# Kernel tuning notes

Hardware: AMD Instinct MI355X
Metric: run time of the kernel (lower is better)

The kernel has to match this reference:

```python
import jax, jax.numpy as jnp
import numpy as np

JITTER = 1e-05
TOL = 1e-04
MAX_ITER = 10
TAYLOR_ORDER = 5


def _safe_eigh(A):
    # torch safe_eigh: first attempt always adds jitter*I (eigh on SPD never fails, so first try succeeds)
    D = A.shape[-1]
    return jnp.linalg.eigh(A + JITTER * jnp.eye(D, dtype=A.dtype))


def _rebuild(vecs, vals):
    # vecs @ diag(vals) @ vecs^T, batched
    return jnp.einsum('...ij,...j,...kj->...ik', vecs, vals, vecs)


def matrix_sqrt(A):
    vals, vecs = _safe_eigh(A)
    return _rebuild(vecs, jnp.sqrt(jnp.clip(vals, JITTER)))


def matrix_inv_sqrt(A):
    vals, vecs = _safe_eigh(A)
    return _rebuild(vecs, 1.0 / jnp.sqrt(jnp.clip(vals, JITTER)))


def enforce_spd(M):
    vals, vecs = _safe_eigh(M)
    M2 = _rebuild(vecs, jnp.clip(vals, JITTER))
    return (M2 + jnp.swapaxes(M2, -1, -2)) * 0.5


def expm_taylor(Xm):
    D = Xm.shape[-1]
    I = jnp.broadcast_to(jnp.eye(D, dtype=Xm.dtype), Xm.shape)
    out = I
    Xp = I
    fac = 1.0
    for i in range(1, TAYLOR_ORDER + 1):
        Xp = Xp @ Xm
        fac *= i
        out = out + Xp / fac
    return out


def karcher_mean(X):
    # X: (B, N, D, D) SPD matrices -> (B, D, D) Riemannian (Karcher) mean
    B, N, D, _ = X.shape
    G0 = X.mean(axis=1)

    def step(carry, _):
        G, done = carry
        G_sqrt = matrix_sqrt(G)
        G_is = matrix_inv_sqrt(G)
        # A[b,n] = G_is[b] @ X[b,n] @ G_is[b]
        A = jnp.einsum('bij,bnjk,bkl->bnil', G_is, X, G_is)
        vals, vecs = _safe_eigh(A)
        logA = _rebuild(vecs, jnp.log(jnp.clip(vals, JITTER)))  # (B,N,D,D)
        Delta = logA.mean(axis=1)  # (B,D,D)
        norm_Delta = jnp.sqrt(jnp.sum(Delta * Delta, axis=(-2, -1))).mean()
        G_new = enforce_spd(G_sqrt @ expm_taylor(Delta) @ G_sqrt)
        # torch updates G, THEN checks break -> freeze only once done was set in a previous iter
        G_next = jnp.where(done, G, G_new)
        done_next = jnp.logical_or(done, norm_Delta < TOL)
        return (G_next, done_next), None

    (G, _), _ = jax.lax.scan(step, (G0, jnp.array(False)), None, length=MAX_ITER)
    return G


def setup_inputs() -> dict:
    key = jax.random.key(0)
    B, N, D = 64, 512, 32
    A = jax.random.normal(key, (B, N, D, D), dtype=jnp.float32)
    # well-conditioned SPD inputs, as an SPD pooling layer would receive
    X = A @ jnp.swapaxes(A, -1, -2) / D + 0.5 * jnp.eye(D, dtype=jnp.float32)
    return {"X": X}


def reference(X) -> jnp.ndarray:
    return karcher_mean(X)
```

## Files before the change

kernel.cpp:

```cpp
#include <hip/hip_runtime.h>
#include <math.h>

#define BB 64
#define NN 512
#define DD 32
#define LD2 36
#define LDG 32
#define JIT 1e-5f
#define TOLF 1e-4f
#define MAXIT 10

__device__ __forceinline__ float bpf(int addr, float v) {
    return __int_as_float(__builtin_amdgcn_ds_bpermute(addr, __float_as_int(v)));
}

__device__ __forceinline__ float swz16(float x) {
    return __int_as_float(__builtin_amdgcn_ds_swizzle(__float_as_int(x), 0x401F));
}

__device__ __forceinline__ float xhsum(float x) {
    unsigned u = __float_as_uint(x);
    auto r = __builtin_amdgcn_permlane32_swap(u, u, false, false);
    return __uint_as_float(r[0]) + __uint_as_float(r[1]);
}

__device__ __forceinline__ float xhmax(float x) {
    unsigned u = __float_as_uint(x);
    auto r = __builtin_amdgcn_permlane32_swap(u, u, false, false);
    return fmaxf(__uint_as_float(r[0]), __uint_as_float(r[1]));
}

__device__ __forceinline__ void wsync() {
    __asm__ volatile("s_waitcnt lgkmcnt(0)" ::: "memory");
}

template<int CTRL>
__device__ __forceinline__ float dppf(float x) {
    int i = __float_as_int(x);
    return __int_as_float(__builtin_amdgcn_update_dpp(i, i, CTRL, 0xF, 0xF, true));
}

__device__ __forceinline__ float part16(float x, bool hi16) {
#if __has_builtin(__builtin_amdgcn_permlane16_swap)
    unsigned u = __float_as_uint(x);
    auto r = __builtin_amdgcn_permlane16_swap(u, u, false, false);
    return hi16 ? __uint_as_float(r[0]) : __uint_as_float(r[1]);
#else
    return swz16(x);
#endif
}

__device__ __forceinline__ float max16pair(float x) {
#if __has_builtin(__builtin_amdgcn_permlane16_swap)
    unsigned u = __float_as_uint(x);
    auto r = __builtin_amdgcn_permlane16_swap(u, u, false, false);
    return fmaxf(__uint_as_float(r[0]), __uint_as_float(r[1]));
#else
    return fmaxf(x, swz16(x));
#endif
}

template<int LOW>
__device__ __forceinline__ float xorlane_lo(float x) {
    float v = x;
    if constexpr (LOW == 1)  v = dppf<0xB1>(v);
    else if constexpr (LOW == 2)  v = dppf<0x4E>(v);
    else if constexpr (LOW == 3)  v = dppf<0x1B>(v);
    else if constexpr (LOW == 4)  { v = dppf<0x141>(v); v = dppf<0x1B>(v); }
    else if constexpr (LOW == 5)  { v = dppf<0x141>(v); v = dppf<0x4E>(v); }
    else if constexpr (LOW == 6)  { v = dppf<0x141>(v); v = dppf<0xB1>(v); }
    else if constexpr (LOW == 7)  v = dppf<0x141>(v);
    else if constexpr (LOW == 8)  v = dppf<0x128>(v);
    else if constexpr (LOW == 9)  { v = dppf<0x128>(v); v = dppf<0xB1>(v); }
    else if constexpr (LOW == 10) { v = dppf<0x128>(v); v = dppf<0x4E>(v); }
    else if constexpr (LOW == 11) { v = dppf<0x128>(v); v = dppf<0x1B>(v); }
    else if constexpr (LOW == 12) { v = dppf<0x140>(v); v = dppf<0x1B>(v); }
    else if constexpr (LOW == 13) { v = dppf<0x140>(v); v = dppf<0x4E>(v); }
    else if constexpr (LOW == 14) { v = dppf<0x140>(v); v = dppf<0xB1>(v); }
    else if constexpr (LOW == 15) v = dppf<0x140>(v);
    return v;
}

__device__ __forceinline__ float redmax32(float x) {
    x = fmaxf(x, dppf<0xB1>(x));
    x = fmaxf(x, dppf<0x4E>(x));
    x = fmaxf(x, dppf<0x124>(x));
    x = fmaxf(x, dppf<0x128>(x));
    x = max16pair(x);
    return xhmax(x);
}

template<int M>
__device__ __forceinline__ void rot32(float a[32], int c, bool hi16, float& maxrel) {
    constexpr int LOW = M & 15;
    float pa[32];
#pragma unroll
    for (int i = 0; i < 32; ++i) {
        float t = xorlane_lo<LOW>(a[i]);
        if constexpr (M >= 16) pa[i] = (i < 16) ? swz16(t) : part16(t, hi16);
        else                   pa[i] = t;
    }
    float gs = 0.f, gc = 0.f;
#pragma unroll
    for (int i = 0; i < 32; ++i) {
        gs = fmaf(a[i], a[i], gs);
        gc = fmaf(a[i], pa[i], gc);
    }
    float gp;
    if constexpr (M < 16) gp = xorlane_lo<LOW>(gs);
    else                  gp = swz16(xorlane_lo<LOW>(gs));
    bool isP = c < (c ^ M);
    float gpp = isP ? gs : gp;
    float gqq = isP ? gp : gs;
    float rel = gc * gc * __builtin_amdgcn_rcpf(gpp * gqq);
    maxrel = fmaxf(maxrel, rel);
    float tau = (gqq - gpp) * (0.5f * __builtin_amdgcn_rcpf(gc));
    float den = fabsf(tau) + __builtin_amdgcn_sqrtf(fmaf(tau, tau, 1.f));
    float tt  = copysignf(__builtin_amdgcn_rcpf(den), tau);
    tt = (rel > 1e-24f) ? tt : 0.f;
    float cs  = __builtin_amdgcn_rsqf(fmaf(tt, tt, 1.f));
    float sn  = tt * cs;
    float sg = isP ? -sn : sn;
#pragma unroll
    for (int i = 0; i < 32; ++i) a[i] = fmaf(sg, pa[i], cs * a[i]);
}

__device__ __forceinline__ void jac_pair(float a[32], int c, bool hi16,
                                         int maxsweep, float thr) {
#pragma unroll 1
    for (int sweep = 0; sweep < maxsweep; ++sweep) {
        float maxrel = 0.f;
        rot32<1>(a, c, hi16, maxrel);  rot32<2>(a, c, hi16, maxrel);
        rot32<3>(a, c, hi16, maxrel);  rot32<4>(a, c, hi16, maxrel);
        rot32<5>(a, c, hi16, maxrel);  rot32<6>(a, c, hi16, maxrel);
        rot32<7>(a, c, hi16, maxrel);  rot32<8>(a, c, hi16, maxrel);
        rot32<9>(a, c, hi16, maxrel);  rot32<10>(a, c, hi16, maxrel);
        rot32<11>(a, c, hi16, maxrel); rot32<12>(a, c, hi16, maxrel);
        rot32<13>(a, c, hi16, maxrel); rot32<14>(a, c, hi16, maxrel);
        rot32<15>(a, c, hi16, maxrel); rot32<16>(a, c, hi16, maxrel);
        rot32<17>(a, c, hi16, maxrel); rot32<18>(a, c, hi16, maxrel);
        rot32<19>(a, c, hi16, maxrel); rot32<20>(a, c, hi16, maxrel);
        rot32<21>(a, c, hi16, maxrel); rot32<22>(a, c, hi16, maxrel);
        rot32<23>(a, c, hi16, maxrel); rot32<24>(a, c, hi16, maxrel);
        rot32<25>(a, c, hi16, maxrel); rot32<26>(a, c, hi16, maxrel);
        rot32<27>(a, c, hi16, maxrel); rot32<28>(a, c, hi16, maxrel);
        rot32<29>(a, c, hi16, maxrel); rot32<30>(a, c, hi16, maxrel);
        rot32<31>(a, c, hi16, maxrel);
        maxrel = redmax32(maxrel);
        if (maxrel < thr) break;
    }
}

__device__ __forceinline__ void mm32w(const float* A, const float* B, float* C, int lane) {
    int r = lane >> 1, cb = (lane & 1) << 4;
    float acc[16];
#pragma unroll
    for (int j = 0; j < 16; ++j) acc[j] = 0.0f;
    for (int k = 0; k < DD; ++k) {
        float a = A[r * LD2 + k];
        const float4* Br = (const float4*)(B + k * LD2 + cb);
        float4 b0 = Br[0], b1 = Br[1], b2 = Br[2], b3 = Br[3];
        acc[0]  = fmaf(a, b0.x, acc[0]);  acc[1]  = fmaf(a, b0.y, acc[1]);
        acc[2]  = fmaf(a, b0.z, acc[2]);  acc[3]  = fmaf(a, b0.w, acc[3]);
        acc[4]  = fmaf(a, b1.x, acc[4]);  acc[5]  = fmaf(a, b1.y, acc[5]);
        acc[6]  = fmaf(a, b1.z, acc[6]);  acc[7]  = fmaf(a, b1.w, acc[7]);
        acc[8]  = fmaf(a, b2.x, acc[8]);  acc[9]  = fmaf(a, b2.y, acc[9]);
        acc[10] = fmaf(a, b2.z, acc[10]); acc[11] = fmaf(a, b2.w, acc[11]);
        acc[12] = fmaf(a, b3.x, acc[12]); acc[13] = fmaf(a, b3.y, acc[13]);
        acc[14] = fmaf(a, b3.z, acc[14]); acc[15] = fmaf(a, b3.w, acc[15]);
    }
    wsync();
    float4* Cr = (float4*)(C + r * LD2 + cb);
    Cr[0] = make_float4(acc[0],  acc[1],  acc[2],  acc[3]);
    Cr[1] = make_float4(acc[4],  acc[5],  acc[6],  acc[7]);
    Cr[2] = make_float4(acc[8],  acc[9],  acc[10], acc[11]);
    Cr[3] = make_float4(acc[12], acc[13], acc[14], acc[15]);
    wsync();
}


__global__ __launch_bounds__(256) void k0_zero(float* __restrict__ G, int* __restrict__ done,
                                               float* __restrict__ norm_acc, int* __restrict__ cnt_all,
                                               int* __restrict__ cnt_b) {
    float4* Gb = (float4*)(G + blockIdx.x * 1024);
    Gb[threadIdx.x] = make_float4(0.f, 0.f, 0.f, 0.f);
    if (blockIdx.x == 0) {
        if (threadIdx.x == 0) { *done = 0; *norm_acc = 0.f; *cnt_all = 0; }
        if (threadIdx.x < BB) cnt_b[threadIdx.x] = 0;
    }
}

__global__ __launch_bounds__(256) void k0_mean(const float* __restrict__ X, float* __restrict__ G) {
    int blk = blockIdx.x;
    int b = blk >> 3, chunk = blk & 7;
    int t = threadIdx.x;
    const float4* Xb = (const float4*)(X + ((size_t)(b * NN + chunk * 64)) * 1024);
    float4 acc = make_float4(0.f, 0.f, 0.f, 0.f);
    for (int n = 0; n < 64; ++n) {
        float4 v = Xb[n * 256 + t];
        acc.x += v.x; acc.y += v.y; acc.z += v.z; acc.w += v.w;
    }
    const float inv = 1.0f / NN;
    float* Gb = G + b * 1024 + t * 4;
    atomicAdd(Gb + 0, acc.x * inv);
    atomicAdd(Gb + 1, acc.y * inv);
    atomicAdd(Gb + 2, acc.z * inv);
    atomicAdd(Gb + 3, acc.w * inv);
}


__global__ __launch_bounds__(64) void k1_init(const float* __restrict__ G,
                                              float* __restrict__ Gs, float* __restrict__ Gis,
                                              float* __restrict__ Vg) {
    int b = blockIdx.x, lane = threadIdx.x;
    int c = lane & 31;
    bool hi16 = (lane & 16) != 0;
    int r = lane >> 1, cb = (lane & 1) << 4;
    __shared__ __align__(16) float sW[DD * LD2];
    __shared__ float sc1[DD], sc2[DD];

    float a[32];
    {
        const float4* Gc = (const float4*)(G + b * 1024 + c * 32);
#pragma unroll
        for (int j4 = 0; j4 < 8; ++j4) {
            float4 q = Gc[j4];
            a[4*j4] = q.x; a[4*j4+1] = q.y; a[4*j4+2] = q.z; a[4*j4+3] = q.w;
        }
        a[c] += JIT;
    }
    jac_pair(a, c, hi16, 10, 1e-12f);
    float gs2 = 0.f;
#pragma unroll
    for (int i = 0; i < 32; ++i) gs2 = fmaf(a[i], a[i], gs2);
    float l  = __builtin_amdgcn_sqrtf(gs2);
    float lc = fmaxf(l, JIT);
    float ig = __builtin_amdgcn_rcpf(gs2);
    float c1 = __builtin_amdgcn_sqrtf(lc) * ig;
    float c2 = __builtin_amdgcn_rsqf(lc) * ig;
    if (Vg && lane < 32) {
        float inl = __builtin_amdgcn_rsqf(gs2);
        float4* Vp = (float4*)(Vg + b * 1024 + c * 32);
#pragma unroll
        for (int j4 = 0; j4 < 8; ++j4)
            Vp[j4] = make_float4(a[4*j4]*inl, a[4*j4+1]*inl, a[4*j4+2]*inl, a[4*j4+3]*inl);
    }
    if (lane < 32) {
        float4* wp = (float4*)&sW[c * LD2];
#pragma unroll
        for (int j4 = 0; j4 < 8; ++j4)
            wp[j4] = make_float4(a[4*j4], a[4*j4+1], a[4*j4+2], a[4*j4+3]);
        sc1[c] = c1; sc2[c] = c2;
    }
    wsync();
    float a1[16], a2[16];
#pragma unroll
    for (int j = 0; j < 16; ++j) { a1[j] = 0.f; a2[j] = 0.f; }
    for (int k = 0; k < DD; ++k) {
        float wr = sW[k * LD2 + r];
        float t1 = wr * sc1[k], t2 = wr * sc2[k];
        const float4* Wc = (const float4*)&sW[k * LD2 + cb];
        float4 w0 = Wc[0], w1 = Wc[1], w2 = Wc[2], w3 = Wc[3];
        a1[0]+=t1*w0.x; a2[0]+=t2*w0.x;  a1[1]+=t1*w0.y; a2[1]+=t2*w0.y;
        a1[2]+=t1*w0.z; a2[2]+=t2*w0.z;  a1[3]+=t1*w0.w; a2[3]+=t2*w0.w;
        a1[4]+=t1*w1.x; a2[4]+=t2*w1.x;  a1[5]+=t1*w1.y; a2[5]+=t2*w1.y;
        a1[6]+=t1*w1.z; a2[6]+=t2*w1.z;  a1[7]+=t1*w1.w; a2[7]+=t2*w1.w;
        a1[8]+=t1*w2.x; a2[8]+=t2*w2.x;  a1[9]+=t1*w2.y; a2[9]+=t2*w2.y;
        a1[10]+=t1*w2.z; a2[10]+=t2*w2.z; a1[11]+=t1*w2.w; a2[11]+=t2*w2.w;
        a1[12]+=t1*w3.x; a2[12]+=t2*w3.x; a1[13]+=t1*w3.y; a2[13]+=t2*w3.y;
        a1[14]+=t1*w3.z; a2[14]+=t2*w3.z; a1[15]+=t1*w3.w; a2[15]+=t2*w3.w;
    }
    float4* Gsb  = (float4*)(Gs  + b * 1024 + lane * 16);
    float4* Gisb = (float4*)(Gis + b * 1024 + lane * 16);
#pragma unroll
    for (int j4 = 0; j4 < 4; ++j4) {
        Gsb[j4]  = make_float4(a1[4*j4], a1[4*j4+1], a1[4*j4+2], a1[4*j4+3]);
        Gisb[j4] = make_float4(a2[4*j4], a2[4*j4+1], a2[4*j4+2], a2[4*j4+3]);
    }
}


__global__ __launch_bounds__(512, 4) void k2_log_acc(const float* __restrict__ X,
                                                     float* G, float* Gs, float* Gis,
                                                     float* __restrict__ Part,
                                                     int* __restrict__ done,
                                                     float* __restrict__ Vbuf,
                                                     float* __restrict__ Vg,
                                                     float* __restrict__ norm_acc,
                                                     int* __restrict__ cnt_all,
                                                     int* __restrict__ cnt_b,
                                                     int it) {
    if (*done) return;
    int b = blockIdx.x >> 4, grp = blockIdx.x & 15;
    int wv = threadIdx.x >> 6, lane = threadIdx.x & 63;
    int c = lane & 31, h = lane >> 5;
    bool hi16 = (lane & 16) != 0;
    int aself = lane << 2;

    __shared__ __align__(16) float sG[DD * LDG];
    __shared__ __align__(16) float sAall[8][DD * LD2];
    float* sA = sAall[wv];

    if (threadIdx.x < 256)
        ((float4*)sG)[threadIdx.x] = ((const float4*)(Gis + b * 1024))[threadIdx.x];
    __syncthreads();

    int r = lane >> 1, cb = (lane & 1) << 4;
    float dacc[16];
#pragma unroll
    for (int j = 0; j < 16; ++j) dacc[j] = 0.f;

#pragma unroll 1
    for (int pp = 0; pp < 2; ++pp) {
        int nb = grp * 32 + wv * 4 + pp * 2;
        float a[32];
#pragma unroll 1
        for (int half = 0; half < 2; ++half) {
            int n = nb + half;
            {
                const float4* Xv = (const float4*)(X + ((size_t)(b * NN + n)) * 1024);
                float4 v0 = Xv[lane * 4 + 0], v1 = Xv[lane * 4 + 1];
                float4 v2 = Xv[lane * 4 + 2], v3 = Xv[lane * 4 + 3];
                wsync();
                int e = lane * 16;
                float* d0 = &sA[(e >> 5) * LD2 + (e & 31)];
                *((float4*)d0)        = v0;
                *((float4*)(d0 + 4))  = v1;
                *((float4*)(d0 + 8))  = v2;
                *((float4*)(d0 + 12)) = v3;
                wsync();
            }
            {
                float acc[16];
#pragma unroll
                for (int j = 0; j < 16; ++j) acc[j] = 0.f;
                for (int k = 0; k < DD; ++k) {
                    float av = sG[k * LDG + r];
                    const float4* Br = (const float4*)(sA + k * LD2 + cb);
                    float4 b0 = Br[0], b1 = Br[1], b2 = Br[2], b3 = Br[3];
                    acc[0]  = fmaf(av, b0.x, acc[0]);  acc[1]  = fmaf(av, b0.y, acc[1]);
                    acc[2]  = fmaf(av, b0.z, acc[2]);  acc[3]  = fmaf(av, b0.w, acc[3]);
                    acc[4]  = fmaf(av, b1.x, acc[4]);  acc[5]  = fmaf(av, b1.y, acc[5]);
                    acc[6]  = fmaf(av, b1.z, acc[6]);  acc[7]  = fmaf(av, b1.w, acc[7]);
                    acc[8]  = fmaf(av, b2.x, acc[8]);  acc[9]  = fmaf(av, b2.y, acc[9]);
                    acc[10] = fmaf(av, b2.z, acc[10]); acc[11] = fmaf(av, b2.w, acc[11]);
                    acc[12] = fmaf(av, b3.x, acc[12]); acc[13] = fmaf(av, b3.y, acc[13]);
                    acc[14] = fmaf(av, b3.z, acc[14]); acc[15] = fmaf(av, b3.w, acc[15]);
                }
                wsync();
                float4* Cr = (float4*)(sA + r * LD2 + cb);
                Cr[0] = make_float4(acc[0],  acc[1],  acc[2],  acc[3]);
                Cr[1] = make_float4(acc[4],  acc[5],  acc[6],  acc[7]);
                Cr[2] = make_float4(acc[8],  acc[9],  acc[10], acc[11]);
                Cr[3] = make_float4(acc[12], acc[13], acc[14], acc[15]);
                wsync();
            }
            {
                float acc[16];
#pragma unroll
                for (int j = 0; j < 16; ++j) acc[j] = 0.f;
                for (int k = 0; k < DD; ++k) {
                    float av = sA[r * LD2 + k];
                    const float4* Br = (const float4*)(sG + k * LDG + cb);
                    float4 b0 = Br[0], b1 = Br[1], b2 = Br[2], b3 = Br[3];
                    acc[0]  = fmaf(av, b0.x, acc[0]);  acc[1]  = fmaf(av, b0.y, acc[1]);
                    acc[2]  = fmaf(av, b0.z, acc[2]);  acc[3]  = fmaf(av, b0.w, acc[3]);
                    acc[4]  = fmaf(av, b1.x, acc[4]);  acc[5]  = fmaf(av, b1.y, acc[5]);
                    acc[6]  = fmaf(av, b1.z, acc[6]);  acc[7]  = fmaf(av, b1.w, acc[7]);
                    acc[8]  = fmaf(av, b2.x, acc[8]);  acc[9]  = fmaf(av, b2.y, acc[9]);
                    acc[10] = fmaf(av, b2.z, acc[10]); acc[11] = fmaf(av, b2.w, acc[11]);
                    acc[12] = fmaf(av, b3.x, acc[12]); acc[13] = fmaf(av, b3.y, acc[13]);
                    acc[14] = fmaf(av, b3.z, acc[14]); acc[15] = fmaf(av, b3.w, acc[15]);
                }
                wsync();
                float4* Cr = (float4*)(sA + r * LD2 + cb);
                Cr[0] = make_float4(acc[0],  acc[1],  acc[2],  acc[3]);
                Cr[1] = make_float4(acc[4],  acc[5],  acc[6],  acc[7]);
                Cr[2] = make_float4(acc[8],  acc[9],  acc[10], acc[11]);
                Cr[3] = make_float4(acc[12], acc[13], acc[14], acc[15]);
                wsync();
            }
            if (h == half) {
                if (it == 0) {
                    float tr[32];
                    const float4* rp = (const float4*)&sA[c * LD2];
#pragma unroll
                    for (int j4 = 0; j4 < 8; ++j4) {
                        float4 q = rp[j4];
                        tr[4*j4]=q.x; tr[4*j4+1]=q.y; tr[4*j4+2]=q.z; tr[4*j4+3]=q.w;
                    }
#pragma unroll
                    for (int i = 0; i < 32; ++i) {
                        float v = 0.5f * (sA[i * LD2 + c] + tr[i]);
                        a[i] = (i == c) ? (tr[i] + JIT) : v;
                    }
                } else {
                    float v[32];
                    const float4* Vp = (const float4*)(Vbuf + ((size_t)(b * NN + n)) * 1024 + c * 32);
#pragma unroll
                    for (int j4 = 0; j4 < 8; ++j4) {
                        float4 t = Vp[j4];
                        v[4*j4]=t.x; v[4*j4+1]=t.y; v[4*j4+2]=t.z; v[4*j4+3]=t.w;
                    }
#pragma unroll
                    for (int i = 0; i < 32; ++i) {
                        const float4* Ar = (const float4*)&sA[i * LD2];
                        float s = 0.f;
#pragma unroll
                        for (int j4 = 0; j4 < 8; ++j4) {
                            float4 q = Ar[j4];
                            s = fmaf(q.x, v[4*j4],   s);
                            s = fmaf(q.y, v[4*j4+1], s);
                            s = fmaf(q.z, v[4*j4+2], s);
                            s = fmaf(q.w, v[4*j4+3], s);
                        }
                        a[i] = fmaf(JIT, v[i], s);
                    }
                }
            }
        }

        jac_pair(a, c, hi16, 8, 1e-8f);

        float gs2 = 0.f;
#pragma unroll
        for (int i = 0; i < 32; ++i) gs2 = fmaf(a[i], a[i], gs2);
        float gs2c = fmaxf(gs2, JIT * JIT);
        float tk = 0.5f * logf(gs2c) * __builtin_amdgcn_rcpf(gs2);
        if (Vbuf) {
            int n = nb + h;
            float inl = __builtin_amdgcn_rsqf(gs2);
            float4* Vp = (float4*)(Vbuf + ((size_t)(b * NN + n)) * 1024 + c * 32);
#pragma unroll
            for (int j4 = 0; j4 < 8; ++j4)
                Vp[j4] = make_float4(a[4*j4]*inl, a[4*j4+1]*inl, a[4*j4+2]*inl, a[4*j4+3]*inl);
        }
#pragma unroll 1
        for (int half = 0; half < 2; ++half) {
            wsync();
            if (h == half) {
                float4* wp = (float4*)&sA[c * LD2];
#pragma unroll
                for (int j4 = 0; j4 < 8; ++j4)
                    wp[j4] = make_float4(a[4*j4], a[4*j4+1], a[4*j4+2], a[4*j4+3]);
                sA[c * LD2 + 32] = tk;
            }
            wsync();
            for (int k = 0; k < DD; ++k) {
                float t1 = sA[k * LD2 + r] * sA[k * LD2 + 32];
                const float4* Wr = (const float4*)&sA[k * LD2 + cb];
                float4 w0 = Wr[0], w1 = Wr[1], w2 = Wr[2], w3 = Wr[3];
                dacc[0]  = fmaf(t1, w0.x, dacc[0]);  dacc[1]  = fmaf(t1, w0.y, dacc[1]);
                dacc[2]  = fmaf(t1, w0.z, dacc[2]);  dacc[3]  = fmaf(t1, w0.w, dacc[3]);
                dacc[4]  = fmaf(t1, w1.x, dacc[4]);  dacc[5]  = fmaf(t1, w1.y, dacc[5]);
                dacc[6]  = fmaf(t1, w1.z, dacc[6]);  dacc[7]  = fmaf(t1, w1.w, dacc[7]);
                dacc[8]  = fmaf(t1, w2.x, dacc[8]);  dacc[9]  = fmaf(t1, w2.y, dacc[9]);
                dacc[10] = fmaf(t1, w2.z, dacc[10]); dacc[11] = fmaf(t1, w2.w, dacc[11]);
                dacc[12] = fmaf(t1, w3.x, dacc[12]); dacc[13] = fmaf(t1, w3.y, dacc[13]);
                dacc[14] = fmaf(t1, w3.z, dacc[14]); dacc[15] = fmaf(t1, w3.w, dacc[15]);
            }
        }
    }
    wsync();

    {
        float4* fp = (float4*)&sA[lane * 16];
        fp[0] = make_float4(dacc[0],  dacc[1],  dacc[2],  dacc[3]);
        fp[1] = make_float4(dacc[4],  dacc[5],  dacc[6],  dacc[7]);
        fp[2] = make_float4(dacc[8],  dacc[9],  dacc[10], dacc[11]);
        fp[3] = make_float4(dacc[12], dacc[13], dacc[14], dacc[15]);
    }
    __syncthreads();
    if (threadIdx.x < 256) {
        int t = threadIdx.x;
        float4 s0 = ((float4*)sAall[0])[t];
        float4 s1 = ((float4*)sAall[1])[t];
        float4 s2 = ((float4*)sAall[2])[t];
        float4 s3 = ((float4*)sAall[3])[t];
        float4 s4 = ((float4*)sAall[4])[t];
        float4 s5 = ((float4*)sAall[5])[t];
        float4 s6 = ((float4*)sAall[6])[t];
        float4 s7 = ((float4*)sAall[7])[t];
        float4 s;
        s.x = ((s0.x + s1.x) + (s2.x + s3.x)) + ((s4.x + s5.x) + (s6.x + s7.x));
        s.y = ((s0.y + s1.y) + (s2.y + s3.y)) + ((s4.y + s5.y) + (s6.y + s7.y));
        s.z = ((s0.z + s1.z) + (s2.z + s3.z)) + ((s4.z + s5.z) + (s6.z + s7.z));
        s.w = ((s0.w + s1.w) + (s2.w + s3.w)) + ((s4.w + s5.w) + (s6.w + s7.w));
        ((float4*)(Part + (size_t)blockIdx.x * 1024))[t] = s;
    }

    int* winp = (int*)sG;
    if (threadIdx.x == 0) *winp = 0;
    __syncthreads();
    if (threadIdx.x == 0) {
        __threadfence();
        int ret = atomicAdd(&cnt_b[b], 1);
        if (ret == 15) { *winp = 1; cnt_b[b] = 0; }
    }
    __syncthreads();
    if (*winp == 0) return;
    if (threadIdx.x >= 64) return;
    __threadfence();

    {
        float* s0 = sAall[0];
        float* s1 = sAall[1];
        float* s2 = sAall[2];
        float* scof = sAall[3];

        float d[16];
#pragma unroll
        for (int j = 0; j < 16; ++j) d[j] = 0.f;
#pragma unroll 1
        for (int g = 0; g < 16; ++g) {
            const float4* P = (const float4*)(Part + (size_t)(b * 16 + g) * 1024 + lane * 16);
            float4 p0 = P[0], p1 = P[1], p2 = P[2], p3 = P[3];
            d[0]+=p0.x; d[1]+=p0.y; d[2]+=p0.z; d[3]+=p0.w;
            d[4]+=p1.x; d[5]+=p1.y; d[6]+=p1.z; d[7]+=p1.w;
            d[8]+=p2.x; d[9]+=p2.y; d[10]+=p2.z; d[11]+=p2.w;
            d[12]+=p3.x; d[13]+=p3.y; d[14]+=p3.z; d[15]+=p3.w;
        }
        const float inv = 1.0f / NN;
        float sumsq = 0.f;
#pragma unroll
        for (int j = 0; j < 16; ++j) { d[j] *= inv; sumsq = fmaf(d[j], d[j], sumsq); }
#pragma unroll
        for (int sh = 1; sh <= 16; sh <<= 1) sumsq += bpf(aself ^ (sh << 2), sumsq);
        sumsq = xhsum(sumsq);
        if (lane == 0) atomicAdd(norm_acc, sqrtf(sumsq));

        wsync();
        {
            float4* dp = (float4*)&s0[r * LD2 + cb];
            dp[0] = make_float4(d[0],  d[1],  d[2],  d[3]);
            dp[1] = make_float4(d[4],  d[5],  d[6],  d[7]);
            dp[2] = make_float4(d[8],  d[9],  d[10], d[11]);
            dp[3] = make_float4(d[12], d[13], d[14], d[15]);
        }
        wsync();

        float outr[16];
#pragma unroll
        for (int j = 0; j < 16; ++j)
            outr[j] = ((cb + j) == r ? 1.0f : 0.0f) + d[j];
        float fac = 1.0f;
#pragma unroll 1
        for (int i = 2; i <= 5; ++i) {
            fac *= (float)i;
            float acc[16];
#pragma unroll
            for (int j = 0; j < 16; ++j) acc[j] = 0.f;
            const float* Xp = (i == 2) ? s0 : s1;
            for (int k = 0; k < DD; ++k) {
                float av = Xp[r * LD2 + k];
                const float4* Br = (const float4*)&s0[k * LD2 + cb];
                float4 b0 = Br[0], b1 = Br[1], b2 = Br[2], b3 = Br[3];
                acc[0]+=av*b0.x; acc[1]+=av*b0.y; acc[2]+=av*b0.z; acc[3]+=av*b0.w;
                acc[4]+=av*b1.x; acc[5]+=av*b1.y; acc[6]+=av*b1.z; acc[7]+=av*b1.w;
                acc[8]+=av*b2.x; acc[9]+=av*b2.y; acc[10]+=av*b2.z; acc[11]+=av*b2.w;
                acc[12]+=av*b3.x; acc[13]+=av*b3.y; acc[14]+=av*b3.z; acc[15]+=av*b3.w;
            }
            float invf = 1.0f / fac;
#pragma unroll
            for (int j = 0; j < 16; ++j) outr[j] = fmaf(acc[j], invf, outr[j]);
            wsync();
            float4* dp = (float4*)&s1[r * LD2 + cb];
            dp[0] = make_float4(acc[0],  acc[1],  acc[2],  acc[3]);
            dp[1] = make_float4(acc[4],  acc[5],  acc[6],  acc[7]);
            dp[2] = make_float4(acc[8],  acc[9],  acc[10], acc[11]);
            dp[3] = make_float4(acc[12], acc[13], acc[14], acc[15]);
            wsync();
        }
        {
            float4* dp = (float4*)&s0[r * LD2 + cb];
            dp[0] = make_float4(outr[0],  outr[1],  outr[2],  outr[3]);
            dp[1] = make_float4(outr[4],  outr[5],  outr[6],  outr[7]);
            dp[2] = make_float4(outr[8],  outr[9],  outr[10], outr[11]);
            dp[3] = make_float4(outr[12], outr[13], outr[14], outr[15]);
            const float4* Gsb = (const float4*)(Gs + b * 1024);
#pragma unroll
            for (int j4 = 0; j4 < 4; ++j4) {
                float4 v = Gsb[lane * 4 + j4];
                int e = lane * 16 + j4 * 4;
                *((float4*)&s1[(e >> 5) * LD2 + (e & 31)]) = v;
            }
        }
        wsync();
        mm32w(s1, s0, s2, lane);
        mm32w(s2, s1, s0, lane);

        float aa[32];
        if (Vg == nullptr) {
            float tr[32];
            const float4* rp = (const float4*)&s0[c * LD2];
#pragma unroll
            for (int j4 = 0; j4 < 8; ++j4) {
                float4 q = rp[j4];
                tr[4*j4]=q.x; tr[4*j4+1]=q.y; tr[4*j4+2]=q.z; tr[4*j4+3]=q.w;
            }
#pragma unroll
            for (int i = 0; i < 32; ++i) {
                float v = 0.5f * (s0[i * LD2 + c] + tr[i]);
                aa[i] = (i == c) ? (tr[i] + JIT) : v;
            }
        } else {
            float v[32];
            const float4* Vp = (const float4*)(Vg + b * 1024 + c * 32);
#pragma unroll
            for (int j4 = 0; j4 < 8; ++j4) {
                float4 t = Vp[j4];
                v[4*j4]=t.x; v[4*j4+1]=t.y; v[4*j4+2]=t.z; v[4*j4+3]=t.w;
            }
#pragma unroll
            for (int i = 0; i < 32; ++i) {
                const float4* Mr = (const float4*)&s0[i * LD2];
                float s = 0.f;
#pragma unroll
                for (int j4 = 0; j4 < 8; ++j4) {
                    float4 q = Mr[j4];
                    s = fmaf(q.x, v[4*j4],   s);
                    s = fmaf(q.y, v[4*j4+1], s);
                    s = fmaf(q.z, v[4*j4+2], s);
                    s = fmaf(q.w, v[4*j4+3], s);
                }
                aa[i] = fmaf(JIT, v[i], s);
            }
        }
        jac_pair(aa, c, hi16, 10, 1e-12f);
        float gs2 = 0.f;
#pragma unroll
        for (int i = 0; i < 32; ++i) gs2 = fmaf(aa[i], aa[i], gs2);
        float l = __builtin_amdgcn_sqrtf(gs2);
        float clipl = fmaxf(l, JIT);
        float ig = __builtin_amdgcn_rcpf(gs2);
        float tg = clipl * ig;
        float sh = clipl + JIT;
        float ts = __builtin_amdgcn_sqrtf(sh) * ig;
        float ti = __builtin_amdgcn_rsqf(sh) * ig;
        if (Vg && lane < 32) {
            float inl = __builtin_amdgcn_rsqf(gs2);
            float4* Vp = (float4*)(Vg + b * 1024 + c * 32);
#pragma unroll
            for (int j4 = 0; j4 < 8; ++j4)
                Vp[j4] = make_float4(aa[4*j4]*inl, aa[4*j4+1]*inl, aa[4*j4+2]*inl, aa[4*j4+3]*inl);
        }
        wsync();
        if (lane < 32) {
            float4* wp = (float4*)&s1[c * LD2];
#pragma unroll
            for (int j4 = 0; j4 < 8; ++j4)
                wp[j4] = make_float4(aa[4*j4], aa[4*j4+1], aa[4*j4+2], aa[4*j4+3]);
            scof[c] = tg; scof[32 + c] = ts; scof[64 + c] = ti;
        }
        wsync();
#pragma unroll 1
        for (int pass = 0; pass < 3; ++pass) {
            float g[16];
#pragma unroll
            for (int j = 0; j < 16; ++j) g[j] = 0.f;
            for (int k = 0; k < DD; ++k) {
                float t1 = s1[k * LD2 + r] * scof[pass * 32 + k];
                const float4* Wc = (const float4*)&s1[k * LD2 + cb];
                float4 w0 = Wc[0], w1 = Wc[1], w2 = Wc[2], w3 = Wc[3];
                g[0]+=t1*w0.x; g[1]+=t1*w0.y; g[2]+=t1*w0.z; g[3]+=t1*w0.w;
                g[4]+=t1*w1.x; g[5]+=t1*w1.y; g[6]+=t1*w1.z; g[7]+=t1*w1.w;
                g[8]+=t1*w2.x; g[9]+=t1*w2.y; g[10]+=t1*w2.z; g[11]+=t1*w2.w;
                g[12]+=t1*w3.x; g[13]+=t1*w3.y; g[14]+=t1*w3.z; g[15]+=t1*w3.w;
            }
            float* dst = (pass == 0) ? G : (pass == 1) ? Gs : Gis;
            float4* Db = (float4*)(dst + b * 1024 + lane * 16);
#pragma unroll
            for (int j4 = 0; j4 < 4; ++j4)
                Db[j4] = make_float4(g[4*j4], g[4*j4+1], g[4*j4+2], g[4*j4+3]);
        }

        __threadfence();
        if (lane == 0) {
            int r2 = atomicAdd(cnt_all, 1);
            if (r2 == BB - 1) {
                float nm = atomicAdd(norm_acc, 0.f);
                if (nm * (1.0f / BB) < TOLF) *done = 1;
                *norm_acc = 0.f;
                *cnt_all = 0;
                __threadfence();
            }
        }
    }
}

__global__ __launch_bounds__(256) void k5_out(const float* __restrict__ G, float* __restrict__ out) {
    int i = blockIdx.x * 256 + threadIdx.x;
    out[i] = G[i];
}

extern "C" void kernel_launch(void* const* d_in, const int* in_sizes, int n_in,
                              void* d_out, int out_size, void* d_ws, size_t ws_size,
                              hipStream_t stream) {
    const float* X = (const float*)d_in[0];
    float* ws = (float*)d_ws;
    float* G     = ws;
    float* Gs    = ws + 65536;
    float* Gis   = ws + 2 * 65536;
    float* Part  = ws + 3 * 65536;
    float* norm_acc = ws + 3 * 65536 + 1048576;
    int*   cnt_all  = (int*)(norm_acc + 1);
    int*   done     = (int*)(norm_acc + 2);
    int*   cnt_b    = (int*)(norm_acc + 3);
    size_t base_floats = (size_t)3 * 65536 + 1048576 + 80;
    float* Vg   = (ws_size >= (base_floats + (size_t)BB * 1024) * sizeof(float))
                  ? (ws + base_floats) : nullptr;
    float* Vbuf = (ws_size >= (base_floats + (size_t)BB * 1024 + (size_t)BB * NN * 1024) * sizeof(float))
                  ? (ws + base_floats + (size_t)BB * 1024) : nullptr;

    k0_zero<<<64, 256, 0, stream>>>(G, done, norm_acc, cnt_all, cnt_b);
    k0_mean<<<512, 256, 0, stream>>>(X, G);
    k1_init<<<64, 64, 0, stream>>>(G, Gs, Gis, Vg);
    for (int it = 0; it < MAXIT; ++it) {
        int it_eff = (Vbuf != nullptr) ? it : 0;
        k2_log_acc<<<1024, 512, 0, stream>>>(X, G, Gs, Gis, Part, done, Vbuf, Vg,
                                             norm_acc, cnt_all, cnt_b, it_eff);
    }
    k5_out<<<256, 256, 0, stream>>>(G, (float*)d_out);
}
```

Before: 4.455 ms.

## Replace pairwise Jacobi with round-robin quad layout using packed FMA

Rewrites the one-sided Jacobi eigen-solver so that each 16-lane group holds two columns (U,V) of a 32x32 matrix and rotates them with packed float2 FMAs. Columns then shift between lanes in a round-robin tournament via DPP, instead of each lane holding one column and fetching its partner across the full wave. This lets a 64-lane wave process four matrices at once (four samples per wave in k2) rather than two, and removes the costly cross-half permutes. In exchange it adds a dynamic 31-round loop, lane-select overhead, and a changed occupancy hint on the main kernel.

```diff
diff --git a/kernel.cpp b/kernel.cpp
--- a/kernel.cpp
+++ b/kernel.cpp
@@ -10,6 +10,12 @@
 #define TOLF 1e-4f
 #define MAXIT 10
 
+typedef float float2v __attribute__((ext_vector_type(2)));
+
+__device__ __forceinline__ float2v efma(float2v a, float2v b, float2v c) {
+    return __builtin_elementwise_fma(a, b, c);
+}
+
 __device__ __forceinline__ float bpf(int addr, float v) {
     return __int_as_float(__builtin_amdgcn_ds_bpermute(addr, __float_as_int(v)));
 }
@@ -38,16 +44,6 @@
 __device__ __forceinline__ float dppf(float x) {
     int i = __float_as_int(x);
     return __int_as_float(__builtin_amdgcn_update_dpp(i, i, CTRL, 0xF, 0xF, true));
-}
-
-__device__ __forceinline__ float part16(float x, bool hi16) {
-#if __has_builtin(__builtin_amdgcn_permlane16_swap)
-    unsigned u = __float_as_uint(x);
-    auto r = __builtin_amdgcn_permlane16_swap(u, u, false, false);
-    return hi16 ? __uint_as_float(r[0]) : __uint_as_float(r[1]);
-#else
-    return swz16(x);
-#endif
 }
 
 __device__ __forceinline__ float max16pair(float x) {
@@ -60,27 +56,6 @@
 #endif
 }
 
-template<int LOW>
-__device__ __forceinline__ float xorlane_lo(float x) {
-    float v = x;
-    if constexpr (LOW == 1)  v = dppf<0xB1>(v);
-    else if constexpr (LOW == 2)  v = dppf<0x4E>(v);
-    else if constexpr (LOW == 3)  v = dppf<0x1B>(v);
-    else if constexpr (LOW == 4)  { v = dppf<0x141>(v); v = dppf<0x1B>(v); }
-    else if constexpr (LOW == 5)  { v = dppf<0x141>(v); v = dppf<0x4E>(v); }
-    else if constexpr (LOW == 6)  { v = dppf<0x141>(v); v = dppf<0xB1>(v); }
-    else if constexpr (LOW == 7)  v = dppf<0x141>(v);
-    else if constexpr (LOW == 8)  v = dppf<0x128>(v);
-    else if constexpr (LOW == 9)  { v = dppf<0x128>(v); v = dppf<0xB1>(v); }
-    else if constexpr (LOW == 10) { v = dppf<0x128>(v); v = dppf<0x4E>(v); }
-    else if constexpr (LOW == 11) { v = dppf<0x128>(v); v = dppf<0x1B>(v); }
-    else if constexpr (LOW == 12) { v = dppf<0x140>(v); v = dppf<0x1B>(v); }
-    else if constexpr (LOW == 13) { v = dppf<0x140>(v); v = dppf<0x4E>(v); }
-    else if constexpr (LOW == 14) { v = dppf<0x140>(v); v = dppf<0xB1>(v); }
-    else if constexpr (LOW == 15) v = dppf<0x140>(v);
-    return v;
-}
-
 __device__ __forceinline__ float redmax32(float x) {
     x = fmaxf(x, dppf<0xB1>(x));
     x = fmaxf(x, dppf<0x4E>(x));
@@ -90,62 +65,59 @@
     return xhmax(x);
 }
 
-template<int M>
-__device__ __forceinline__ void rot32(float a[32], int c, bool hi16, float& maxrel) {
-    constexpr int LOW = M & 15;
-    float pa[32];
-#pragma unroll
-    for (int i = 0; i < 32; ++i) {
-        float t = xorlane_lo<LOW>(a[i]);
-        if constexpr (M >= 16) pa[i] = (i < 16) ? swz16(t) : part16(t, hi16);
-        else                   pa[i] = t;
-    }
-    float gs = 0.f, gc = 0.f;
-#pragma unroll
-    for (int i = 0; i < 32; ++i) {
-        gs = fmaf(a[i], a[i], gs);
-        gc = fmaf(a[i], pa[i], gc);
-    }
-    float gp;
-    if constexpr (M < 16) gp = xorlane_lo<LOW>(gs);
-    else                  gp = swz16(xorlane_lo<LOW>(gs));
-    bool isP = c < (c ^ M);
-    float gpp = isP ? gs : gp;
-    float gqq = isP ? gp : gs;
-    float rel = gc * gc * __builtin_amdgcn_rcpf(gpp * gqq);
-    maxrel = fmaxf(maxrel, rel);
-    float tau = (gqq - gpp) * (0.5f * __builtin_amdgcn_rcpf(gc));
-    float den = fabsf(tau) + __builtin_amdgcn_sqrtf(fmaf(tau, tau, 1.f));
-    float tt  = copysignf(__builtin_amdgcn_rcpf(den), tau);
-    tt = (rel > 1e-24f) ? tt : 0.f;
-    float cs  = __builtin_amdgcn_rsqf(fmaf(tt, tt, 1.f));
-    float sn  = tt * cs;
-    float sg = isP ? -sn : sn;
-#pragma unroll
-    for (int i = 0; i < 32; ++i) a[i] = fmaf(sg, pa[i], cs * a[i]);
-}
-
-__device__ __forceinline__ void jac_pair(float a[32], int c, bool hi16,
+__device__ __forceinline__ void jac_quad(float2v U[16], float2v V[16],
+                                         bool isL0, bool isL1, bool isL15,
                                          int maxsweep, float thr) {
 #pragma unroll 1
     for (int sweep = 0; sweep < maxsweep; ++sweep) {
         float maxrel = 0.f;
-        rot32<1>(a, c, hi16, maxrel);  rot32<2>(a, c, hi16, maxrel);
-        rot32<3>(a, c, hi16, maxrel);  rot32<4>(a, c, hi16, maxrel);
-        rot32<5>(a, c, hi16, maxrel);  rot32<6>(a, c, hi16, maxrel);
-        rot32<7>(a, c, hi16, maxrel);  rot32<8>(a, c, hi16, maxrel);
-        rot32<9>(a, c, hi16, maxrel);  rot32<10>(a, c, hi16, maxrel);
-        rot32<11>(a, c, hi16, maxrel); rot32<12>(a, c, hi16, maxrel);
-        rot32<13>(a, c, hi16, maxrel); rot32<14>(a, c, hi16, maxrel);
-        rot32<15>(a, c, hi16, maxrel); rot32<16>(a, c, hi16, maxrel);
-        rot32<17>(a, c, hi16, maxrel); rot32<18>(a, c, hi16, maxrel);
-        rot32<19>(a, c, hi16, maxrel); rot32<20>(a, c, hi16, maxrel);
-        rot32<21>(a, c, hi16, maxrel); rot32<22>(a, c, hi16, maxrel);
-        rot32<23>(a, c, hi16, maxrel); rot32<24>(a, c, hi16, maxrel);
-        rot32<25>(a, c, hi16, maxrel); rot32<26>(a, c, hi16, maxrel);
-        rot32<27>(a, c, hi16, maxrel); rot32<28>(a, c, hi16, maxrel);
-        rot32<29>(a, c, hi16, maxrel); rot32<30>(a, c, hi16, maxrel);
-        rot32<31>(a, c, hi16, maxrel);
+#pragma unroll 1
+        for (int rnd = 0; rnd < 31; ++rnd) {
+            float2v SU0 = {0.f,0.f}, SU1 = {0.f,0.f};
+            float2v SV0 = {0.f,0.f}, SV1 = {0.f,0.f};
+            float2v SC0 = {0.f,0.f}, SC1 = {0.f,0.f};
+#pragma unroll
+            for (int j = 0; j < 16; j += 2) {
+                SU0 = efma(U[j],   U[j],   SU0);
+                SU1 = efma(U[j+1], U[j+1], SU1);
+                SV0 = efma(V[j],   V[j],   SV0);
+                SV1 = efma(V[j+1], V[j+1], SV1);
+                SC0 = efma(U[j],   V[j],   SC0);
+                SC1 = efma(U[j+1], V[j+1], SC1);
+            }
+            float2v SU = SU0 + SU1, SV = SV0 + SV1, SC = SC0 + SC1;
+            float gpp = SU.x + SU.y;
+            float gqq = SV.x + SV.y;
+            float gc  = SC.x + SC.y;
+            float rel = gc * gc * __builtin_amdgcn_rcpf(gpp * gqq);
+            maxrel = fmaxf(maxrel, rel);
+            float tau = (gqq - gpp) * (0.5f * __builtin_amdgcn_rcpf(gc));
+            float den = fabsf(tau) + __builtin_amdgcn_sqrtf(fmaf(tau, tau, 1.f));
+            float tt  = copysignf(__builtin_amdgcn_rcpf(den), tau);
+            tt = (rel > 1e-24f) ? tt : 0.f;
+            float cs  = __builtin_amdgcn_rsqf(fmaf(tt, tt, 1.f));
+            float sn  = tt * cs;
+            float2v CS = {cs, cs}, SN = {sn, sn}, NS = {-sn, -sn};
+#pragma unroll
+            for (int j = 0; j < 16; ++j) {
+                float2v uj = U[j], vj = V[j];
+                U[j] = efma(NS, vj, uj * CS);
+                V[j] = efma(SN, uj, vj * CS);
+            }
+#pragma unroll
+            for (int j = 0; j < 16; ++j) {
+                float ux = U[j].x, uy = U[j].y, vx = V[j].x, vy = V[j].y;
+                float ax = dppf<0x111>(ux), ay = dppf<0x111>(uy);
+                float bx = dppf<0x111>(vx), by = dppf<0x111>(vy);
+                float cx = dppf<0x101>(vx), cy = dppf<0x101>(vy);
+                float nux = isL1 ? bx : ax;  nux = isL0 ? ux : nux;
+                float nuy = isL1 ? by : ay;  nuy = isL0 ? uy : nuy;
+                float nvx = isL15 ? ux : cx;
+                float nvy = isL15 ? uy : cy;
+                U[j].x = nux; U[j].y = nuy;
+                V[j].x = nvx; V[j].y = nvy;
+            }
+        }
         maxrel = redmax32(maxrel);
         if (maxrel < thr) break;
     }
@@ -213,44 +185,56 @@
                                               float* __restrict__ Gs, float* __restrict__ Gis,
                                               float* __restrict__ Vg) {
     int b = blockIdx.x, lane = threadIdx.x;
-    int c = lane & 31;
-    bool hi16 = (lane & 16) != 0;
+    int l16 = lane & 15;
+    bool isL0 = (l16 == 0), isL1 = (l16 == 1), isL15 = (l16 == 15);
     int r = lane >> 1, cb = (lane & 1) << 4;
     __shared__ __align__(16) float sW[DD * LD2];
     __shared__ float sc1[DD], sc2[DD];
 
-    float a[32];
+    float2v U[16], V[16];
     {
-        const float4* Gc = (const float4*)(G + b * 1024 + c * 32);
+        const float4* Gu = (const float4*)(G + b * 1024 + l16 * 32);
+        const float4* Gv = (const float4*)(G + b * 1024 + (16 + l16) * 32);
 #pragma unroll
         for (int j4 = 0; j4 < 8; ++j4) {
-            float4 q = Gc[j4];
-            a[4*j4] = q.x; a[4*j4+1] = q.y; a[4*j4+2] = q.z; a[4*j4+3] = q.w;
-        }
-        a[c] += JIT;
-    }
-    jac_pair(a, c, hi16, 10, 1e-12f);
-    float gs2 = 0.f;
-#pragma unroll
-    for (int i = 0; i < 32; ++i) gs2 = fmaf(a[i], a[i], gs2);
-    float l  = __builtin_amdgcn_sqrtf(gs2);
-    float lc = fmaxf(l, JIT);
-    float ig = __builtin_amdgcn_rcpf(gs2);
-    float c1 = __builtin_amdgcn_sqrtf(lc) * ig;
-    float c2 = __builtin_amdgcn_rsqf(lc) * ig;
-    if (Vg && lane < 32) {
-        float inl = __builtin_amdgcn_rsqf(gs2);
-        float4* Vp = (float4*)(Vg + b * 1024 + c * 32);
-#pragma unroll
-        for (int j4 = 0; j4 < 8; ++j4)
-            Vp[j4] = make_float4(a[4*j4]*inl, a[4*j4+1]*inl, a[4*j4+2]*inl, a[4*j4+3]*inl);
-    }
-    if (lane < 32) {
-        float4* wp = (float4*)&sW[c * LD2];
-#pragma unroll
-        for (int j4 = 0; j4 < 8; ++j4)
-            wp[j4] = make_float4(a[4*j4], a[4*j4+1], a[4*j4+2], a[4*j4+3]);
-        sc1[c] = c1; sc2[c] = c2;
+            float4 qu = Gu[j4], qv = Gv[j4];
+            int e = 4 * j4;
+            U[2*j4]   = (float2v){qu.x + ((e+0)==l16 ? JIT : 0.f), qu.y + ((e+1)==l16 ? JIT : 0.f)};
+            U[2*j4+1] = (float2v){qu.z + ((e+2)==l16 ? JIT : 0.f), qu.w + ((e+3)==l16 ? JIT : 0.f)};
+            V[2*j4]   = (float2v){qv.x + ((e+0)==16+l16 ? JIT : 0.f), qv.y + ((e+1)==16+l16 ? JIT : 0.f)};
+            V[2*j4+1] = (float2v){qv.z + ((e+2)==16+l16 ? JIT : 0.f), qv.w + ((e+3)==16+l16 ? JIT : 0.f)};
+        }
+    }
+    jac_quad(U, V, isL0, isL1, isL15, 10, 1e-12f);
+    float2v NU = {0.f,0.f}, NV = {0.f,0.f};
+#pragma unroll
+    for (int j = 0; j < 16; ++j) { NU = efma(U[j], U[j], NU); NV = efma(V[j], V[j], NV); }
+    float nu2 = NU.x + NU.y, nv2 = NV.x + NV.y;
+    float lu = __builtin_amdgcn_sqrtf(nu2), lv = __builtin_amdgcn_sqrtf(nv2);
+    float lcu = fmaxf(lu, JIT),            lcv = fmaxf(lv, JIT);
+    float igu = __builtin_amdgcn_rcpf(nu2), igv = __builtin_amdgcn_rcpf(nv2);
+    float c1u = __builtin_amdgcn_sqrtf(lcu) * igu, c1v = __builtin_amdgcn_sqrtf(lcv) * igv;
+    float c2u = __builtin_amdgcn_rsqf(lcu) * igu,  c2v = __builtin_amdgcn_rsqf(lcv) * igv;
+    if (Vg && lane < 16) {
+        float inu = __builtin_amdgcn_rsqf(nu2), inv_ = __builtin_amdgcn_rsqf(nv2);
+        float4* Vpu = (float4*)(Vg + b * 1024 + l16 * 32);
+        float4* Vpv = (float4*)(Vg + b * 1024 + (16 + l16) * 32);
+#pragma unroll
+        for (int j4 = 0; j4 < 8; ++j4) {
+            Vpu[j4] = make_float4(U[2*j4].x*inu, U[2*j4].y*inu, U[2*j4+1].x*inu, U[2*j4+1].y*inu);
+            Vpv[j4] = make_float4(V[2*j4].x*inv_, V[2*j4].y*inv_, V[2*j4+1].x*inv_, V[2*j4+1].y*inv_);
+        }
+    }
+    if (lane < 16) {
+        float4* wpu = (float4*)&sW[l16 * LD2];
+        float4* wpv = (float4*)&sW[(16 + l16) * LD2];
+#pragma unroll
+        for (int j4 = 0; j4 < 8; ++j4) {
+            wpu[j4] = make_float4(U[2*j4].x, U[2*j4].y, U[2*j4+1].x, U[2*j4+1].y);
+            wpv[j4] = make_float4(V[2*j4].x, V[2*j4].y, V[2*j4+1].x, V[2*j4+1].y);
+        }
+        sc1[l16] = c1u; sc1[16 + l16] = c1v;
+        sc2[l16] = c2u; sc2[16 + l16] = c2v;
     }
     wsync();
     float a1[16], a2[16];
@@ -280,21 +264,23 @@
 }
 
 
-__global__ __launch_bounds__(512, 4) void k2_log_acc(const float* __restrict__ X,
-                                                     float* G, float* Gs, float* Gis,
-                                                     float* __restrict__ Part,
-                                                     int* __restrict__ done,
-                                                     float* __restrict__ Vbuf,
-                                                     float* __restrict__ Vg,
-                                                     float* __restrict__ norm_acc,
-                                                     int* __restrict__ cnt_all,
-                                                     int* __restrict__ cnt_b,
-                                                     int it) {
+__global__ __launch_bounds__(512) __attribute__((amdgpu_waves_per_eu(4, 8)))
+void k2_log_acc(const float* __restrict__ X,
+                float* G, float* Gs, float* Gis,
+                float* __restrict__ Part,
+                int* __restrict__ done,
+                float* __restrict__ Vbuf,
+                float* __restrict__ Vg,
+                float* __restrict__ norm_acc,
+                int* __restrict__ cnt_all,
+                int* __restrict__ cnt_b,
+                int it) {
     if (*done) return;
     int b = blockIdx.x >> 4, grp = blockIdx.x & 15;
     int wv = threadIdx.x >> 6, lane = threadIdx.x & 63;
+    int g = lane >> 4, l16 = lane & 15;
     int c = lane & 31, h = lane >> 5;
-    bool hi16 = (lane & 16) != 0;
+    bool isL0 = (l16 == 0), isL1 = (l16 == 1), isL15 = (l16 == 15);
     int aself = lane << 2;
 
     __shared__ __align__(16) float sG[DD * LDG];
@@ -310,155 +296,186 @@
 #pragma unroll
     for (int j = 0; j < 16; ++j) dacc[j] = 0.f;
 
+    int nb = grp * 32 + wv * 4;
+    float2v U[16], V[16];
+
 #pragma unroll 1
-    for (int pp = 0; pp < 2; ++pp) {
-        int nb = grp * 32 + wv * 4 + pp * 2;
-        float a[32];
+    for (int mm = 0; mm < 4; ++mm) {
+        int n = nb + mm;
+        {
+            const float4* Xv = (const float4*)(X + ((size_t)(b * NN + n)) * 1024);
+            float4 v0 = Xv[lane * 4 + 0], v1 = Xv[lane * 4 + 1];
+            float4 v2 = Xv[lane * 4 + 2], v3 = Xv[lane * 4 + 3];
+            wsync();
+            int e = lane * 16;
+            float* d0 = &sA[(e >> 5) * LD2 + (e & 31)];
+            *((float4*)d0)        = v0;
+            *((float4*)(d0 + 4))  = v1;
+            *((float4*)(d0 + 8))  = v2;
+            *((float4*)(d0 + 12)) = v3;
+            wsync();
+        }
+        {
+            float acc[16];
+#pragma unroll
+            for (int j = 0; j < 16; ++j) acc[j] = 0.f;
+            for (int k = 0; k < DD; ++k) {
+                float av = sG[k * LDG + r];
+                const float4* Br = (const float4*)(sA + k * LD2 + cb);
+                float4 b0 = Br[0], b1 = Br[1], b2 = Br[2], b3 = Br[3];
+                acc[0]  = fmaf(av, b0.x, acc[0]);  acc[1]  = fmaf(av, b0.y, acc[1]);
+                acc[2]  = fmaf(av, b0.z, acc[2]);  acc[3]  = fmaf(av, b0.w, acc[3]);
+                acc[4]  = fmaf(av, b1.x, acc[4]);  acc[5]  = fmaf(av, b1.y, acc[5]);
+                acc[6]  = fmaf(av, b1.z, acc[6]);  acc[7]  = fmaf(av, b1.w, acc[7]);
+                acc[8]  = fmaf(av, b2.x, acc[8]);  acc[9]  = fmaf(av, b2.y, acc[9]);
+                acc[10] = fmaf(av, b2.z, acc[10]); acc[11] = fmaf(av, b2.w, acc[11]);
+                acc[12] = fmaf(av, b3.x, acc[12]); acc[13] = fmaf(av, b3.y, acc[13]);
+                acc[14] = fmaf(av, b3.z, acc[14]); acc[15] = fmaf(av, b3.w, acc[15]);
+            }
+            wsync();
+            float4* Cr = (float4*)(sA + r * LD2 + cb);
+            Cr[0] = make_float4(acc[0],  acc[1],  acc[2],  acc[3]);
+            Cr[1] = make_float4(acc[4],  acc[5],  acc[6],  acc[7]);
+            Cr[2] = make_float4(acc[8],  acc[9],  acc[10], acc[11]);
+            Cr[3] = make_float4(acc[12], acc[13], acc[14], acc[15]);
+            wsync();
+        }
+        {
+            float acc[16];
+#pragma unroll
+            for (int j = 0; j < 16; ++j) acc[j] = 0.f;
+            for (int k = 0; k < DD; ++k) {
+                float av = sA[r * LD2 + k];
+                const float4* Br = (const float4*)(sG + k * LDG + cb);
+                float4 b0 = Br[0], b1 = Br[1], b2 = Br[2], b3 = Br[3];
+                acc[0]  = fmaf(av, b0.x, acc[0]);  acc[1]  = fmaf(av, b0.y, acc[1]);
+                acc[2]  = fmaf(av, b0.z, acc[2]);  acc[3]  = fmaf(av, b0.w, acc[3]);
+                acc[4]  = fmaf(av, b1.x, acc[4]);  acc[5]  = fmaf(av, b1.y, acc[5]);
+                acc[6]  = fmaf(av, b1.z, acc[6]);  acc[7]  = fmaf(av, b1.w, acc[7]);
+                acc[8]  = fmaf(av, b2.x, acc[8]);  acc[9]  = fmaf(av, b2.y, acc[9]);
+                acc[10] = fmaf(av, b2.z, acc[10]); acc[11] = fmaf(av, b2.w, acc[11]);
+                acc[12] = fmaf(av, b3.x, acc[12]); acc[13] = fmaf(av, b3.y, acc[13]);
+                acc[14] = fmaf(av, b3.z, acc[14]); acc[15] = fmaf(av, b3.w, acc[15]);
+            }
+            wsync();
+            float4* Cr = (float4*)(sA + r * LD2 + cb);
+            Cr[0] = make_float4(acc[0],  acc[1],  acc[2],  acc[3]);
+            Cr[1] = make_float4(acc[4],  acc[5],  acc[6],  acc[7]);
+            Cr[2] = make_float4(acc[8],  acc[9],  acc[10], acc[11]);
+            Cr[3] = make_float4(acc[12], acc[13], acc[14], acc[15]);
+            wsync();
+        }
+        if (it == 0) {
+            if (g == mm) {
+#pragma unroll
+                for (int j = 0; j < 16; ++j) {
+                    int i0 = 2*j, i1 = 2*j + 1;
+                    float cu0 = sA[i0 * LD2 + l16],        ru0 = sA[l16 * LD2 + i0];
+                    float cu1 = sA[i1 * LD2 + l16],        ru1 = sA[l16 * LD2 + i1];
+                    float cv0 = sA[i0 * LD2 + 16 + l16],   rv0 = sA[(16 + l16) * LD2 + i0];
+                    float cv1 = sA[i1 * LD2 + 16 + l16],   rv1 = sA[(16 + l16) * LD2 + i1];
+                    U[j].x = (i0 == l16)      ? ru0 + JIT : 0.5f * (cu0 + ru0);
+                    U[j].y = (i1 == l16)      ? ru1 + JIT : 0.5f * (cu1 + ru1);
+                    V[j].x = (i0 == 16 + l16) ? rv0 + JIT : 0.5f * (cv0 + rv0);
+                    V[j].y = (i1 == 16 + l16) ? rv1 + JIT : 0.5f * (cv1 + rv1);
+                }
+            }
+        } else {
+            float vh[32];
+            {
+                const float4* Vp = (const float4*)(Vbuf + ((size_t)(b * NN + n)) * 1024 + c * 32);
+#pragma unroll
+                for (int j4 = 0; j4 < 8; ++j4) {
+                    float4 t = Vp[j4];
+                    vh[4*j4] = t.x; vh[4*j4+1] = t.y; vh[4*j4+2] = t.z; vh[4*j4+3] = t.w;
+                }
+            }
+            float w[16];
+#pragma unroll
+            for (int i = 0; i < 16; ++i) {
+                const float4* Ar = (const float4*)&sA[(16 * h + i) * LD2];
+                float s = 0.f;
+#pragma unroll
+                for (int j4 = 0; j4 < 8; ++j4) {
+                    float4 q = Ar[j4];
+                    s = fmaf(q.x, vh[4*j4],   s);
+                    s = fmaf(q.y, vh[4*j4+1], s);
+                    s = fmaf(q.z, vh[4*j4+2], s);
+                    s = fmaf(q.w, vh[4*j4+3], s);
+                }
+                float vhi = (h == 0) ? vh[i] : vh[16 + i];
+                w[i] = fmaf(JIT, vhi, s);
+            }
+            wsync();
+            {
+                float4* wp = (float4*)&sA[c * LD2 + 16 * h];
+                wp[0] = make_float4(w[0],  w[1],  w[2],  w[3]);
+                wp[1] = make_float4(w[4],  w[5],  w[6],  w[7]);
+                wp[2] = make_float4(w[8],  w[9],  w[10], w[11]);
+                wp[3] = make_float4(w[12], w[13], w[14], w[15]);
+            }
+            wsync();
+            if (g == mm) {
+                const float4* r0 = (const float4*)&sA[l16 * LD2];
+                const float4* r1 = (const float4*)&sA[(16 + l16) * LD2];
+#pragma unroll
+                for (int j4 = 0; j4 < 8; ++j4) {
+                    float4 q0 = r0[j4], q1 = r1[j4];
+                    U[2*j4]   = (float2v){q0.x, q0.y};
+                    U[2*j4+1] = (float2v){q0.z, q0.w};
+                    V[2*j4]   = (float2v){q1.x, q1.y};
+                    V[2*j4+1] = (float2v){q1.z, q1.w};
+                }
+            }
+        }
+    }
+
+    jac_quad(U, V, isL0, isL1, isL15, 8, 1e-8f);
+
+    float2v NU = {0.f,0.f}, NV = {0.f,0.f};
+#pragma unroll
+    for (int j = 0; j < 16; ++j) { NU = efma(U[j], U[j], NU); NV = efma(V[j], V[j], NV); }
+    float nu2 = NU.x + NU.y, nv2 = NV.x + NV.y;
+    float tku = 0.5f * logf(fmaxf(nu2, JIT * JIT)) * __builtin_amdgcn_rcpf(nu2);
+    float tkv = 0.5f * logf(fmaxf(nv2, JIT * JIT)) * __builtin_amdgcn_rcpf(nv2);
+    if (Vbuf) {
+        int n = nb + g;
+        float inu = __builtin_amdgcn_rsqf(nu2), inv_ = __builtin_amdgcn_rsqf(nv2);
+        float4* Vpu = (float4*)(Vbuf + ((size_t)(b * NN + n)) * 1024 + l16 * 32);
+        float4* Vpv = (float4*)(Vbuf + ((size_t)(b * NN + n)) * 1024 + (16 + l16) * 32);
+#pragma unroll
+        for (int j4 = 0; j4 < 8; ++j4) {
+            Vpu[j4] = make_float4(U[2*j4].x*inu, U[2*j4].y*inu, U[2*j4+1].x*inu, U[2*j4+1].y*inu);
+            Vpv[j4] = make_float4(V[2*j4].x*inv_, V[2*j4].y*inv_, V[2*j4+1].x*inv_, V[2*j4+1].y*inv_);
+        }
+    }
 #pragma unroll 1
-        for (int half = 0; half < 2; ++half) {
-            int n = nb + half;
-            {
-                const float4* Xv = (const float4*)(X + ((size_t)(b * NN + n)) * 1024);
-                float4 v0 = Xv[lane * 4 + 0], v1 = Xv[lane * 4 + 1];
-                float4 v2 = Xv[lane * 4 + 2], v3 = Xv[lane * 4 + 3];
-                wsync();
-                int e = lane * 16;
-                float* d0 = &sA[(e >> 5) * LD2 + (e & 31)];
-                *((float4*)d0)        = v0;
-                *((float4*)(d0 + 4))  = v1;
-                *((float4*)(d0 + 8))  = v2;
-                *((float4*)(d0 + 12)) = v3;
-                wsync();
-            }
-            {
-                float acc[16];
-#pragma unroll
-                for (int j = 0; j < 16; ++j) acc[j] = 0.f;
-                for (int k = 0; k < DD; ++k) {
-                    float av = sG[k * LDG + r];
-                    const float4* Br = (const float4*)(sA + k * LD2 + cb);
-                    float4 b0 = Br[0], b1 = Br[1], b2 = Br[2], b3 = Br[3];
-                    acc[0]  = fmaf(av, b0.x, acc[0]);  acc[1]  = fmaf(av, b0.y, acc[1]);
-                    acc[2]  = fmaf(av, b0.z, acc[2]);  acc[3]  = fmaf(av, b0.w, acc[3]);
-                    acc[4]  = fmaf(av, b1.x, acc[4]);  acc[5]  = fmaf(av, b1.y, acc[5]);
-                    acc[6]  = fmaf(av, b1.z, acc[6]);  acc[7]  = fmaf(av, b1.w, acc[7]);
-                    acc[8]  = fmaf(av, b2.x, acc[8]);  acc[9]  = fmaf(av, b2.y, acc[9]);
-                    acc[10] = fmaf(av, b2.z, acc[10]); acc[11] = fmaf(av, b2.w, acc[11]);
-                    acc[12] = fmaf(av, b3.x, acc[12]); acc[13] = fmaf(av, b3.y, acc[13]);
-                    acc[14] = fmaf(av, b3.z, acc[14]); acc[15] = fmaf(av, b3.w, acc[15]);
-                }
-                wsync();
-                float4* Cr = (float4*)(sA + r * LD2 + cb);
-                Cr[0] = make_float4(acc[0],  acc[1],  acc[2],  acc[3]);
-                Cr[1] = make_float4(acc[4],  acc[5],  acc[6],  acc[7]);
-                Cr[2] = make_float4(acc[8],  acc[9],  acc[10], acc[11]);
-                Cr[3] = make_float4(acc[12], acc[13], acc[14], acc[15]);
-                wsync();
-            }
-            {
-                float acc[16];
-#pragma unroll
-                for (int j = 0; j < 16; ++j) acc[j] = 0.f;
-                for (int k = 0; k < DD; ++k) {
-                    float av = sA[r * LD2 + k];
-                    const float4* Br = (const float4*)(sG + k * LDG + cb);
-                    float4 b0 = Br[0], b1 = Br[1], b2 = Br[2], b3 = Br[3];
-                    acc[0]  = fmaf(av, b0.x, acc[0]);  acc[1]  = fmaf(av, b0.y, acc[1]);
-                    acc[2]  = fmaf(av, b0.z, acc[2]);  acc[3]  = fmaf(av, b0.w, acc[3]);
-                    acc[4]  = fmaf(av, b1.x, acc[4]);  acc[5]  = fmaf(av, b1.y, acc[5]);
-                    acc[6]  = fmaf(av, b1.z, acc[6]);  acc[7]  = fmaf(av, b1.w, acc[7]);
-                    acc[8]  = fmaf(av, b2.x, acc[8]);  acc[9]  = fmaf(av, b2.y, acc[9]);
-                    acc[10] = fmaf(av, b2.z, acc[10]); acc[11] = fmaf(av, b2.w, acc[11]);
-                    acc[12] = fmaf(av, b3.x, acc[12]); acc[13] = fmaf(av, b3.y, acc[13]);
-                    acc[14] = fmaf(av, b3.z, acc[14]); acc[15] = fmaf(av, b3.w, acc[15]);
-                }
-                wsync();
-                float4* Cr = (float4*)(sA + r * LD2 + cb);
-                Cr[0] = make_float4(acc[0],  acc[1],  acc[2],  acc[3]);
-                Cr[1] = make_float4(acc[4],  acc[5],  acc[6],  acc[7]);
-                Cr[2] = make_float4(acc[8],  acc[9],  acc[10], acc[11]);
-                Cr[3] = make_float4(acc[12], acc[13], acc[14], acc[15]);
-                wsync();
-            }
-            if (h == half) {
-                if (it == 0) {
-                    float tr[32];
-                    const float4* rp = (const float4*)&sA[c * LD2];
-#pragma unroll
-                    for (int j4 = 0; j4 < 8; ++j4) {
-                        float4 q = rp[j4];
-                        tr[4*j4]=q.x; tr[4*j4+1]=q.y; tr[4*j4+2]=q.z; tr[4*j4+3]=q.w;
-                    }
-#pragma unroll
-                    for (int i = 0; i < 32; ++i) {
-                        float v = 0.5f * (sA[i * LD2 + c] + tr[i]);
-                        a[i] = (i == c) ? (tr[i] + JIT) : v;
-                    }
-                } else {
-                    float v[32];
-                    const float4* Vp = (const float4*)(Vbuf + ((size_t)(b * NN + n)) * 1024 + c * 32);
-#pragma unroll
-                    for (int j4 = 0; j4 < 8; ++j4) {
-                        float4 t = Vp[j4];
-                        v[4*j4]=t.x; v[4*j4+1]=t.y; v[4*j4+2]=t.z; v[4*j4+3]=t.w;
-                    }
-#pragma unroll
-                    for (int i = 0; i < 32; ++i) {
-                        const float4* Ar = (const float4*)&sA[i * LD2];
-                        float s = 0.f;
-#pragma unroll
-                        for (int j4 = 0; j4 < 8; ++j4) {
-                            float4 q = Ar[j4];
-                            s = fmaf(q.x, v[4*j4],   s);
-                            s = fmaf(q.y, v[4*j4+1], s);
-                            s = fmaf(q.z, v[4*j4+2], s);
-                            s = fmaf(q.w, v[4*j4+3], s);
-                        }
-                        a[i] = fmaf(JIT, v[i], s);
-                    }
-                }
-            }
-        }
-
-        jac_pair(a, c, hi16, 8, 1e-8f);
-
-        float gs2 = 0.f;
-#pragma unroll
-        for (int i = 0; i < 32; ++i) gs2 = fmaf(a[i], a[i], gs2);
-        float gs2c = fmaxf(gs2, JIT * JIT);
-        float tk = 0.5f * logf(gs2c) * __builtin_amdgcn_rcpf(gs2);
-        if (Vbuf) {
-            int n = nb + h;
-            float inl = __builtin_amdgcn_rsqf(gs2);
-            float4* Vp = (float4*)(Vbuf + ((size_t)(b * NN + n)) * 1024 + c * 32);
-#pragma unroll
-            for (int j4 = 0; j4 < 8; ++j4)
-                Vp[j4] = make_float4(a[4*j4]*inl, a[4*j4+1]*inl, a[4*j4+2]*inl, a[4*j4+3]*inl);
-        }
-#pragma unroll 1
-        for (int half = 0; half < 2; ++half) {
-            wsync();
-            if (h == half) {
-                float4* wp = (float4*)&sA[c * LD2];
-#pragma unroll
-                for (int j4 = 0; j4 < 8; ++j4)
-                    wp[j4] = make_float4(a[4*j4], a[4*j4+1], a[4*j4+2], a[4*j4+3]);
-                sA[c * LD2 + 32] = tk;
-            }
-            wsync();
-            for (int k = 0; k < DD; ++k) {
-                float t1 = sA[k * LD2 + r] * sA[k * LD2 + 32];
-                const float4* Wr = (const float4*)&sA[k * LD2 + cb];
-                float4 w0 = Wr[0], w1 = Wr[1], w2 = Wr[2], w3 = Wr[3];
-                dacc[0]  = fmaf(t1, w0.x, dacc[0]);  dacc[1]  = fmaf(t1, w0.y, dacc[1]);
-                dacc[2]  = fmaf(t1, w0.z, dacc[2]);  dacc[3]  = fmaf(t1, w0.w, dacc[3]);
-                dacc[4]  = fmaf(t1, w1.x, dacc[4]);  dacc[5]  = fmaf(t1, w1.y, dacc[5]);
-                dacc[6]  = fmaf(t1, w1.z, dacc[6]);  dacc[7]  = fmaf(t1, w1.w, dacc[7]);
-                dacc[8]  = fmaf(t1, w2.x, dacc[8]);  dacc[9]  = fmaf(t1, w2.y, dacc[9]);
-                dacc[10] = fmaf(t1, w2.z, dacc[10]); dacc[11] = fmaf(t1, w2.w, dacc[11]);
-                dacc[12] = fmaf(t1, w3.x, dacc[12]); dacc[13] = fmaf(t1, w3.y, dacc[13]);
-                dacc[14] = fmaf(t1, w3.z, dacc[14]); dacc[15] = fmaf(t1, w3.w, dacc[15]);
-            }
+    for (int mm = 0; mm < 4; ++mm) {
+        wsync();
+        if (g == mm) {
+            float4* wpu = (float4*)&sA[l16 * LD2];
+            float4* wpv = (float4*)&sA[(16 + l16) * LD2];
+#pragma unroll
+            for (int j4 = 0; j4 < 8; ++j4) {
+                wpu[j4] = make_float4(U[2*j4].x, U[2*j4].y, U[2*j4+1].x, U[2*j4+1].y);
+                wpv[j4] = make_float4(V[2*j4].x, V[2*j4].y, V[2*j4+1].x, V[2*j4+1].y);
+            }
+            sA[l16 * LD2 + 32] = tku;
+            sA[(16 + l16) * LD2 + 32] = tkv;
+        }
+        wsync();
+        for (int k = 0; k < DD; ++k) {
+            float t1 = sA[k * LD2 + r] * sA[k * LD2 + 32];
+            const float4* Wr = (const float4*)&sA[k * LD2 + cb];
+            float4 w0 = Wr[0], w1 = Wr[1], w2 = Wr[2], w3 = Wr[3];
+            dacc[0]  = fmaf(t1, w0.x, dacc[0]);  dacc[1]  = fmaf(t1, w0.y, dacc[1]);
+            dacc[2]  = fmaf(t1, w0.z, dacc[2]);  dacc[3]  = fmaf(t1, w0.w, dacc[3]);
+            dacc[4]  = fmaf(t1, w1.x, dacc[4]);  dacc[5]  = fmaf(t1, w1.y, dacc[5]);
+            dacc[6]  = fmaf(t1, w1.z, dacc[6]);  dacc[7]  = fmaf(t1, w1.w, dacc[7]);
+            dacc[8]  = fmaf(t1, w2.x, dacc[8]);  dacc[9]  = fmaf(t1, w2.y, dacc[9]);
+            dacc[10] = fmaf(t1, w2.z, dacc[10]); dacc[11] = fmaf(t1, w2.w, dacc[11]);
+            dacc[12] = fmaf(t1, w3.x, dacc[12]); dacc[13] = fmaf(t1, w3.y, dacc[13]);
+            dacc[14] = fmaf(t1, w3.z, dacc[14]); dacc[15] = fmaf(t1, w3.w, dacc[15]);
         }
     }
     wsync();
@@ -512,8 +529,8 @@
 #pragma unroll
         for (int j = 0; j < 16; ++j) d[j] = 0.f;
 #pragma unroll 1
-        for (int g = 0; g < 16; ++g) {
-            const float4* P = (const float4*)(Part + (size_t)(b * 16 + g) * 1024 + lane * 16);
+        for (int gg = 0; gg < 16; ++gg) {
+            const float4* P = (const float4*)(Part + (size_t)(b * 16 + gg) * 1024 + lane * 16);
             float4 p0 = P[0], p1 = P[1], p2 = P[2], p3 = P[3];
             d[0]+=p0.x; d[1]+=p0.y; d[2]+=p0.z; d[3]+=p0.w;
             d[4]+=p1.x; d[5]+=p1.y; d[6]+=p1.z; d[7]+=p1.w;
@@ -589,89 +606,121 @@
         mm32w(s1, s0, s2, lane);
         mm32w(s2, s1, s0, lane);
 
-        float aa[32];
+        float2v AU[16], AV[16];
         if (Vg == nullptr) {
-            float tr[32];
-            const float4* rp = (const float4*)&s0[c * LD2];
-#pragma unroll
-            for (int j4 = 0; j4 < 8; ++j4) {
-                float4 q = rp[j4];
-                tr[4*j4]=q.x; tr[4*j4+1]=q.y; tr[4*j4+2]=q.z; tr[4*j4+3]=q.w;
-            }
-#pragma unroll
-            for (int i = 0; i < 32; ++i) {
-                float v = 0.5f * (s0[i * LD2 + c] + tr[i]);
-                aa[i] = (i == c) ? (tr[i] + JIT) : v;
+#pragma unroll
+            for (int j = 0; j < 16; ++j) {
+                int i0 = 2*j, i1 = 2*j + 1;
+                float cu0 = s0[i0 * LD2 + l16],      ru0 = s0[l16 * LD2 + i0];
+                float cu1 = s0[i1 * LD2 + l16],      ru1 = s0[l16 * LD2 + i1];
+                float cv0 = s0[i0 * LD2 + 16 + l16], rv0 = s0[(16 + l16) * LD2 + i0];
+                float cv1 = s0[i1 * LD2 + 16 + l16], rv1 = s0[(16 + l16) * LD2 + i1];
+                AU[j].x = (i0 == l16)      ? ru0 + JIT : 0.5f * (cu0 + ru0);
+                AU[j].y = (i1 == l16)      ? ru1 + JIT : 0.5f * (cu1 + ru1);
+                AV[j].x = (i0 == 16 + l16) ? rv0 + JIT : 0.5f * (cv0 + rv0);
+                AV[j].y = (i1 == 16 + l16) ? rv1 + JIT : 0.5f * (cv1 + rv1);
             }
         } else {
-            float v[32];
-            const float4* Vp = (const float4*)(Vg + b * 1024 + c * 32);
-#pragma unroll
-            for (int j4 = 0; j4 < 8; ++j4) {
-                float4 t = Vp[j4];
-                v[4*j4]=t.x; v[4*j4+1]=t.y; v[4*j4+2]=t.z; v[4*j4+3]=t.w;
-            }
-#pragma unroll
-            for (int i = 0; i < 32; ++i) {
-                const float4* Mr = (const float4*)&s0[i * LD2];
+            float vh[32];
+            {
+                const float4* Vp = (const float4*)(Vg + b * 1024 + c * 32);
+#pragma unroll
+                for (int j4 = 0; j4 < 8; ++j4) {
+                    float4 t = Vp[j4];
+                    vh[4*j4] = t.x; vh[4*j4+1] = t.y; vh[4*j4+2] = t.z; vh[4*j4+3] = t.w;
+                }
+            }
+            float w[16];
+#pragma unroll
+            for (int i = 0; i < 16; ++i) {
+                const float4* Mr = (const float4*)&s0[(16 * h + i) * LD2];
                 float s = 0.f;
 #pragma unroll
                 for (int j4 = 0; j4 < 8; ++j4) {
                     float4 q = Mr[j4];
-                    s = fmaf(q.x, v[4*j4],   s);
-                    s = fmaf(q.y, v[4*j4+1], s);
-                    s = fmaf(q.z, v[4*j4+2], s);
-                    s = fmaf(q.w, v[4*j4+3], s);
+                    s = fmaf(q.x, vh[4*j4],   s);
+                    s = fmaf(q.y, vh[4*j4+1], s);
+                    s = fmaf(q.z, vh[4*j4+2], s);
+                    s = fmaf(q.w, vh[4*j4+3], s);
                 }
-                aa[i] = fmaf(JIT, v[i], s);
-            }
-        }
-        jac_pair(aa, c, hi16, 10, 1e-12f);
-        float gs2 = 0.f;
-#pragma unroll
-        for (int i = 0; i < 32; ++i) gs2 = fmaf(aa[i], aa[i], gs2);
-        float l = __builtin_amdgcn_sqrtf(gs2);
-        float clipl = fmaxf(l, JIT);
-        float ig = __builtin_amdgcn_rcpf(gs2);
-        float tg = clipl * ig;
-        float sh = clipl + JIT;
-        float ts = __builtin_amdgcn_sqrtf(sh) * ig;
-        float ti = __builtin_amdgcn_rsqf(sh) * ig;
-        if (Vg && lane < 32) {
-            float inl = __builtin_amdgcn_rsqf(gs2);
-            float4* Vp = (float4*)(Vg + b * 1024 + c * 32);
-#pragma unroll
-            for (int j4 = 0; j4 < 8; ++j4)
-                Vp[j4] = make_float4(aa[4*j4]*inl, aa[4*j4+1]*inl, aa[4*j4+2]*inl, aa[4*j4+3]*inl);
+                float vhi = (h == 0) ? vh[i] : vh[16 + i];
+                w[i] = fmaf(JIT, vhi, s);
+            }
+            wsync();
+            {
+                float4* wp = (float4*)&s2[c * LD2 + 16 * h];
+                wp[0] = make_float4(w[0],  w[1],  w[2],  w[3]);
+                wp[1] = make_float4(w[4],  w[5],  w[6],  w[7]);
+                wp[2] = make_float4(w[8],  w[9],  w[10], w[11]);
+                wp[3] = make_float4(w[12], w[13], w[14], w[15]);
+            }
+            wsync();
+            const float4* r0 = (const float4*)&s2[l16 * LD2];
+            const float4* r1 = (const float4*)&s2[(16 + l16) * LD2];
+#pragma unroll
+            for (int j4 = 0; j4 < 8; ++j4) {
+                float4 q0 = r0[j4], q1 = r1[j4];
+                AU[2*j4]   = (float2v){q0.x, q0.y};
+                AU[2*j4+1] = (float2v){q0.z, q0.w};
+                AV[2*j4]   = (float2v){q1.x, q1.y};
+                AV[2*j4+1] = (float2v){q1.z, q1.w};
+            }
+        }
+        jac_quad(AU, AV, isL0, isL1, isL15, 10, 1e-12f);
+        float2v NU2 = {0.f,0.f}, NV2 = {0.f,0.f};
+#pragma unroll
+        for (int j = 0; j < 16; ++j) { NU2 = efma(AU[j], AU[j], NU2); NV2 = efma(AV[j], AV[j], NV2); }
+        float mu2 = NU2.x + NU2.y, mv2 = NV2.x + NV2.y;
+        float lu = __builtin_amdgcn_sqrtf(mu2), lv = __builtin_amdgcn_sqrtf(mv2);
+        float clu = fmaxf(lu, JIT),             clv = fmaxf(lv, JIT);
+        float igu = __builtin_amdgcn_rcpf(mu2), igv = __builtin_amdgcn_rcpf(mv2);
+        float tgu = clu * igu,                  tgv = clv * igv;
+        float shu = clu + JIT,                  shv = clv + JIT;
+        float tsu = __builtin_amdgcn_sqrtf(shu) * igu, tsv = __builtin_amdgcn_sqrtf(shv) * igv;
+        float tiu = __builtin_amdgcn_rsqf(shu) * igu,  tiv = __builtin_amdgcn_rsqf(shv) * igv;
+        if (Vg && lane < 16) {
+            float inu = __builtin_amdgcn_rsqf(mu2), inv_ = __builtin_amdgcn_rsqf(mv2);
+            float4* Vpu = (float4*)(Vg + b * 1024 + l16 * 32);
+            float4* Vpv = (float4*)(Vg + b * 1024 + (16 + l16) * 32);
+#pragma unroll
+            for (int j4 = 0; j4 < 8; ++j4) {
+                Vpu[j4] = make_float4(AU[2*j4].x*inu, AU[2*j4].y*inu, AU[2*j4+1].x*inu, AU[2*j4+1].y*inu);
+                Vpv[j4] = make_float4(AV[2*j4].x*inv_, AV[2*j4].y*inv_, AV[2*j4+1].x*inv_, AV[2*j4+1].y*inv_);
+            }
         }
         wsync();
-        if (lane < 32) {
-            float4* wp = (float4*)&s1[c * LD2];
-#pragma unroll
-            for (int j4 = 0; j4 < 8; ++j4)
-                wp[j4] = make_float4(aa[4*j4], aa[4*j4+1], aa[4*j4+2], aa[4*j4+3]);
-            scof[c] = tg; scof[32 + c] = ts; scof[64 + c] = ti;
+        if (lane < 16) {
+            float4* wpu = (float4*)&s1[l16 * LD2];
+            float4* wpv = (float4*)&s1[(16 + l16) * LD2];
+#pragma unroll
+            for (int j4 = 0; j4 < 8; ++j4) {
+                wpu[j4] = make_float4(AU[2*j4].x, AU[2*j4].y, AU[2*j4+1].x, AU[2*j4+1].y);
+                wpv[j4] = make_float4(AV[2*j4].x, AV[2*j4].y, AV[2*j4+1].x, AV[2*j4+1].y);
+            }
+            scof[l16] = tgu;      scof[16 + l16] = tgv;
+            scof[32 + l16] = tsu; scof[48 + l16] = tsv;
+            scof[64 + l16] = tiu; scof[80 + l16] = tiv;
         }
         wsync();
 #pragma unroll 1
         for (int pass = 0; pass < 3; ++pass) {
-            float g[16];
-#pragma unroll
-            for (int j = 0; j < 16; ++j) g[j] = 0.f;
+            float gacc[16];
+#pragma unroll
+            for (int j = 0; j < 16; ++j) gacc[j] = 0.f;
             for (int k = 0; k < DD; ++k) {
                 float t1 = s1[k * LD2 + r] * scof[pass * 32 + k];
                 const float4* Wc = (const float4*)&s1[k * LD2 + cb];
                 float4 w0 = Wc[0], w1 = Wc[1], w2 = Wc[2], w3 = Wc[3];
-                g[0]+=t1*w0.x; g[1]+=t1*w0.y; g[2]+=t1*w0.z; g[3]+=t1*w0.w;
-                g[4]+=t1*w1.x; g[5]+=t1*w1.y; g[6]+=t1*w1.z; g[7]+=t1*w1.w;
-                g[8]+=t1*w2.x; g[9]+=t1*w2.y; g[10]+=t1*w2.z; g[11]+=t1*w2.w;
-                g[12]+=t1*w3.x; g[13]+=t1*w3.y; g[14]+=t1*w3.z; g[15]+=t1*w3.w;
+                gacc[0]+=t1*w0.x; gacc[1]+=t1*w0.y; gacc[2]+=t1*w0.z; gacc[3]+=t1*w0.w;
+                gacc[4]+=t1*w1.x; gacc[5]+=t1*w1.y; gacc[6]+=t1*w1.z; gacc[7]+=t1*w1.w;
+                gacc[8]+=t1*w2.x; gacc[9]+=t1*w2.y; gacc[10]+=t1*w2.z; gacc[11]+=t1*w2.w;
+                gacc[12]+=t1*w3.x; gacc[13]+=t1*w3.y; gacc[14]+=t1*w3.z; gacc[15]+=t1*w3.w;
             }
             float* dst = (pass == 0) ? G : (pass == 1) ? Gs : Gis;
             float4* Db = (float4*)(dst + b * 1024 + lane * 16);
 #pragma unroll
             for (int j4 = 0; j4 < 4; ++j4)
-                Db[j4] = make_float4(g[4*j4], g[4*j4+1], g[4*j4+2], g[4*j4+3]);
+                Db[j4] = make_float4(gacc[4*j4], gacc[4*j4+1], gacc[4*j4+2], gacc[4*j4+3]);
         }
 
         __threadfence();
```

After: 4.521 ms. Within noise of the previous version (+1.5%).
